# Optimization experiments

Measured on AMD Instinct MI355X. Metric: run time of the kernel, lower is better.

Reference implementation:

```python
import math
import jax, jax.numpy as jnp
import numpy as np

_MAX_CELL_MULTIPLES = 100000


def _grid_bounds(cell, cutoff, r1, r2):
    """Static (concrete) grid bounds, mirroring the module's a_max/b_max/c_max."""
    cell = np.asarray(cell, dtype=np.float64)
    dr = np.asarray(r2, dtype=np.float64) - np.asarray(r1, dtype=np.float64)
    a, b, c = cell[0], cell[1], cell[2]
    vol = abs(float(np.dot(a, np.cross(b, c))))

    def nmax(u, v):
        cr = np.cross(u, v)
        ln = float(np.linalg.norm(cr))
        d = abs(float(np.dot(dr, cr / ln)))
        return min(int(math.floor((cutoff + d) / vol * ln)), _MAX_CELL_MULTIPLES)

    return nmax(b, c), nmax(a, c), nmax(a, b)


def _candidate_grid(a_max, b_max, c_max):
    ii, jj, kk = jnp.meshgrid(
        jnp.arange(-a_max, a_max + 1),
        jnp.arange(-b_max, b_max + 1),
        jnp.arange(-c_max, c_max + 1),
        indexing="ij",
    )
    # [N,3] int32, ordered exactly like the original triple nested loop (i outer, k inner)
    return jnp.stack([ii.ravel(), jj.ravel(), kk.ravel()], axis=-1).astype(jnp.int32)


def setup_inputs() -> dict:
    key = jax.random.key(0)
    k1, k2 = jax.random.split(key)
    cell = jnp.array([[2.0, 0.0, 0.0], [0.1, 2.0, 0.0], [0.1, 0.1, 2.0]], dtype=jnp.float32)
    cutoff = jnp.float32(200.0)
    r1 = jax.random.normal(k1, (3,), dtype=jnp.float32)
    r2 = jax.random.normal(k2, (3,), dtype=jnp.float32)
    return {"cell": cell, "cutoff": cutoff, "r1": r1, "r2": r2}


def reference(cell, cutoff, r1, r2):
    # Grid extents are concrete (computed from host values), so shapes are static.
    a_max, b_max, c_max = _grid_bounds(cell, float(cutoff), r1, r2)
    ijk = _candidate_grid(a_max, b_max, c_max)  # [N,3] int32
    dr = r2 - r1
    # displacement = i*a + j*b + k*c for every lattice image, vectorized as a GEMM
    disp = ijk.astype(cell.dtype) @ cell  # [N,3]
    out_vec = disp + dr  # [N,3]
    mask = jnp.sum(out_vec * out_vec, axis=-1) < cutoff * cutoff  # [N]
    # Padded/masked equivalent of the original's variable-length compaction:
    # rows with mask==False are zeroed instead of removed (static shapes for jit).
    vectors = jnp.where(mask[:, None], out_vec, jnp.zeros((), out_vec.dtype))
    cell_indices = jnp.where(mask[:, None], ijk, jnp.zeros((), ijk.dtype))
    return vectors, cell_indices, mask
```

## Files before the change

### kernel.cpp

```cpp
#include <hip/hip_runtime.h>
#include <stdint.h>

struct Params {
  int a_max, b_max, c_max;
  uint32_t Dj, Dk;
  uint64_t Mj, Mk;
};

__device__ __forceinline__ int iabs_(int x) { return x < 0 ? -x : x; }

__device__ __forceinline__ int nmax_ref(double u0, double u1, double u2,
                                        double v0, double v1, double v2,
                                        double dr0, double dr1, double dr2,
                                        double co, double vol) {
#pragma clang fp contract(off)
  double x0 = u1 * v2 - u2 * v1;
  double x1 = u2 * v0 - u0 * v2;
  double x2 = u0 * v1 - u1 * v0;
  double ln = sqrt((x0 * x0 + x1 * x1) + x2 * x2);
  double d  = fabs((dr0 * (x0 / ln) + dr1 * (x1 / ln)) + dr2 * (x2 / ln));
  double f  = floor((co + d) / vol * ln);
  long long n = (long long)f;
  if (n > 100000) n = 100000;
  return (int)n;
}

__global__ void setup_kernel(const float* __restrict__ cell,
                             const float* __restrict__ cutoff,
                             const float* __restrict__ r1,
                             const float* __restrict__ r2,
                             Params* __restrict__ p, int N) {
#pragma clang fp contract(off)
  double a0 = cell[0], a1 = cell[1], a2 = cell[2];
  double b0 = cell[3], b1 = cell[4], b2 = cell[5];
  double c0 = cell[6], c1 = cell[7], c2 = cell[8];
  double dr0 = (double)r2[0] - (double)r1[0];
  double dr1 = (double)r2[1] - (double)r1[1];
  double dr2 = (double)r2[2] - (double)r1[2];
  double co  = (double)cutoff[0];

  double bc0 = b1 * c2 - b2 * c1;
  double bc1 = b2 * c0 - b0 * c2;
  double bc2 = b0 * c1 - b1 * c0;
  double vol = fabs((a0 * bc0 + a1 * bc1) + a2 * bc2);

  int am = nmax_ref(b0, b1, b2, c0, c1, c2, dr0, dr1, dr2, co, vol);
  int bm = nmax_ref(a0, a1, a2, c0, c1, c2, dr0, dr1, dr2, co, vol);
  int cm = nmax_ref(a0, a1, a2, b0, b1, b2, dr0, dr1, dr2, co, vol);

  int fa = am, fb = bm, fc = cm;
  bool found = ((long long)(2 * am + 1) * (2 * bm + 1) * (2 * cm + 1) == (long long)N);
  for (int r = 1; r <= 3 && !found; ++r)
    for (int da = -1; da <= 1 && !found; ++da)
      for (int db = -1; db <= 1 && !found; ++db)
        for (int dc = -1; dc <= 1 && !found; ++dc) {
          if (iabs_(da) + iabs_(db) + iabs_(dc) != r) continue;
          long long A = am + da, B = bm + db, C = cm + dc;
          if (A < 0 || B < 0 || C < 0) continue;
          long long P = (2 * A + 1) * (2 * B + 1) * (2 * C + 1);
          if (P == (long long)N) { fa = (int)A; fb = (int)B; fc = (int)C; found = true; }
        }

  p->a_max = fa; p->b_max = fb; p->c_max = fc;
  uint32_t Dk = (uint32_t)(2 * fc + 1);
  uint32_t Dj = (uint32_t)(2 * fb + 1) * Dk;
  p->Dk = Dk; p->Dj = Dj;
  p->Mj = ((1ULL << 47) / Dj) + 1;
  p->Mk = ((1ULL << 47) / Dk) + 1;
}

__global__ __launch_bounds__(256) void periodic_main(
    const float* __restrict__ cell, const float* __restrict__ cutoff,
    const float* __restrict__ r1, const float* __restrict__ r2,
    const Params* __restrict__ p, float* __restrict__ out, int N) {
  int n = blockIdx.x * 256 + threadIdx.x;
  if (n >= N) return;

  const int am = p->a_max, bm = p->b_max, cm = p->c_max;
  const uint32_t Dj = p->Dj, Dk = p->Dk;
  const uint64_t Mj = p->Mj, Mk = p->Mk;

  uint32_t un  = (uint32_t)n;
  uint32_t qi  = (uint32_t)(((uint64_t)un * Mj) >> 47);
  uint32_t rem = un - qi * Dj;
  uint32_t qj  = (uint32_t)(((uint64_t)rem * Mk) >> 47);
  uint32_t qk  = rem - qj * Dk;

  float fi = (float)((int)qi - am);
  float fj = (float)((int)qj - bm);
  float fk = (float)((int)qk - cm);

  float ax = cell[0], ay = cell[1], az = cell[2];
  float bx = cell[3], by = cell[4], bz = cell[5];
  float cx = cell[6], cy = cell[7], cz = cell[8];
  float drx = r2[0] - r1[0], dry = r2[1] - r1[1], drz = r2[2] - r1[2];

  float vx = fmaf(fk, cx, fmaf(fj, bx, fi * ax)) + drx;
  float vy = fmaf(fk, cy, fmaf(fj, by, fi * ay)) + dry;
  float vz = fmaf(fk, cz, fmaf(fj, bz, fi * az)) + drz;

  float s  = fmaf(vz, vz, fmaf(vy, vy, vx * vx));
  float co = cutoff[0];
  bool  m  = s < co * co;

  float vxo = m ? vx : 0.f, vyo = m ? vy : 0.f, vzo = m ? vz : 0.f;
  float fio = m ? fi : 0.f, fjo = m ? fj : 0.f, fko = m ? fk : 0.f;

  size_t base = (size_t)3 * (size_t)n;
  size_t N3   = (size_t)3 * (size_t)N;
  __builtin_nontemporal_store(vxo, out + base + 0);
  __builtin_nontemporal_store(vyo, out + base + 1);
  __builtin_nontemporal_store(vzo, out + base + 2);
  __builtin_nontemporal_store(fio, out + N3 + base + 0);
  __builtin_nontemporal_store(fjo, out + N3 + base + 1);
  __builtin_nontemporal_store(fko, out + N3 + base + 2);
  __builtin_nontemporal_store(m ? 1.0f : 0.0f, out + 2 * N3 + (size_t)n);
}

extern "C" void kernel_launch(void* const* d_in, const int* in_sizes, int n_in,
                              void* d_out, int out_size, void* d_ws, size_t ws_size,
                              hipStream_t stream) {
  const float* cell   = (const float*)d_in[0];
  const float* cutoff = (const float*)d_in[1];
  const float* r1     = (const float*)d_in[2];
  const float* r2     = (const float*)d_in[3];
  float* out = (float*)d_out;

  int N = out_size / 7;
  Params* p = (Params*)d_ws;

  setup_kernel<<<1, 1, 0, stream>>>(cell, cutoff, r1, r2, p, N);
  int blocks = (N + 255) / 256;
  periodic_main<<<blocks, 256, 0, stream>>>(cell, cutoff, r1, r2, p, out, N);
}
```

Measured before the change: 254.6 us.

## Stage outputs in shared memory and write coalesced float4 stores

Each block now handles 1024 points with 4 per thread and writes the strided 3-component results into shared memory first. It then copies them to global memory as aligned float4 vector stores, with scalar head and tail handling for misaligned segment offsets. This replaces the stride-3 scalar nontemporal stores with wide coalesced writes. The cost is shared memory use, a block barrier, and the loss of nontemporal hints.

```diff
diff --git a/kernel.cpp b/kernel.cpp
--- a/kernel.cpp
+++ b/kernel.cpp
@@ -73,48 +73,101 @@
     const float* __restrict__ cell, const float* __restrict__ cutoff,
     const float* __restrict__ r1, const float* __restrict__ r2,
     const Params* __restrict__ p, float* __restrict__ out, int N) {
-  int n = blockIdx.x * 256 + threadIdx.x;
-  if (n >= N) return;
+  __shared__ __align__(16) float s_vec[3 * 1024];
+  __shared__ __align__(16) float s_idx[4 + 3 * 1024];
+  __shared__ __align__(16) float s_msk[4 + 1024];
+
+  const int tid = threadIdx.x;
+  const int n0  = blockIdx.x << 10;
 
   const int am = p->a_max, bm = p->b_max, cm = p->c_max;
   const uint32_t Dj = p->Dj, Dk = p->Dk;
   const uint64_t Mj = p->Mj, Mk = p->Mk;
 
-  uint32_t un  = (uint32_t)n;
-  uint32_t qi  = (uint32_t)(((uint64_t)un * Mj) >> 47);
-  uint32_t rem = un - qi * Dj;
-  uint32_t qj  = (uint32_t)(((uint64_t)rem * Mk) >> 47);
-  uint32_t qk  = rem - qj * Dk;
+  const float ax = cell[0], ay = cell[1], az = cell[2];
+  const float bx = cell[3], by = cell[4], bz = cell[5];
+  const float cx = cell[6], cy = cell[7], cz = cell[8];
+  const float drx = r2[0] - r1[0], dry = r2[1] - r1[1], drz = r2[2] - r1[2];
+  const float co  = cutoff[0];
+  const float co2 = co * co;
 
-  float fi = (float)((int)qi - am);
-  float fj = (float)((int)qj - bm);
-  float fk = (float)((int)qk - cm);
+  const size_t NN = (size_t)N;
+  const size_t gA = (size_t)3 * (size_t)n0;
+  const size_t gB = (size_t)3 * NN + (size_t)3 * (size_t)n0;
+  const size_t gC = (size_t)6 * NN + (size_t)n0;
+  const int s1 = (int)(gB & 3);
+  const int s2 = (int)(gC & 3);
 
-  float ax = cell[0], ay = cell[1], az = cell[2];
-  float bx = cell[3], by = cell[4], bz = cell[5];
-  float cx = cell[6], cy = cell[7], cz = cell[8];
-  float drx = r2[0] - r1[0], dry = r2[1] - r1[1], drz = r2[2] - r1[2];
+#pragma unroll
+  for (int u = 0; u < 4; ++u) {
+    const int pt = tid + (u << 8);
+    const int n  = n0 + pt;
+    if (n < N) {
+      uint32_t un  = (uint32_t)n;
+      uint32_t qi  = (uint32_t)(((uint64_t)un * Mj) >> 47);
+      uint32_t rem = un - qi * Dj;
+      uint32_t qj  = (uint32_t)(((uint64_t)rem * Mk) >> 47);
+      uint32_t qk  = rem - qj * Dk;
 
-  float vx = fmaf(fk, cx, fmaf(fj, bx, fi * ax)) + drx;
-  float vy = fmaf(fk, cy, fmaf(fj, by, fi * ay)) + dry;
-  float vz = fmaf(fk, cz, fmaf(fj, bz, fi * az)) + drz;
+      float fi = (float)((int)qi - am);
+      float fj = (float)((int)qj - bm);
+      float fk = (float)((int)qk - cm);
 
-  float s  = fmaf(vz, vz, fmaf(vy, vy, vx * vx));
-  float co = cutoff[0];
-  bool  m  = s < co * co;
+      float vx = fmaf(fk, cx, fmaf(fj, bx, fi * ax)) + drx;
+      float vy = fmaf(fk, cy, fmaf(fj, by, fi * ay)) + dry;
+      float vz = fmaf(fk, cz, fmaf(fj, bz, fi * az)) + drz;
 
-  float vxo = m ? vx : 0.f, vyo = m ? vy : 0.f, vzo = m ? vz : 0.f;
-  float fio = m ? fi : 0.f, fjo = m ? fj : 0.f, fko = m ? fk : 0.f;
+      float s = fmaf(vz, vz, fmaf(vy, vy, vx * vx));
+      bool  m = s < co2;
 
-  size_t base = (size_t)3 * (size_t)n;
-  size_t N3   = (size_t)3 * (size_t)N;
-  __builtin_nontemporal_store(vxo, out + base + 0);
-  __builtin_nontemporal_store(vyo, out + base + 1);
-  __builtin_nontemporal_store(vzo, out + base + 2);
-  __builtin_nontemporal_store(fio, out + N3 + base + 0);
-  __builtin_nontemporal_store(fjo, out + N3 + base + 1);
-  __builtin_nontemporal_store(fko, out + N3 + base + 2);
-  __builtin_nontemporal_store(m ? 1.0f : 0.0f, out + 2 * N3 + (size_t)n);
+      int b3 = 3 * pt;
+      s_vec[b3 + 0]      = m ? vx : 0.f;
+      s_vec[b3 + 1]      = m ? vy : 0.f;
+      s_vec[b3 + 2]      = m ? vz : 0.f;
+      s_idx[s1 + b3 + 0] = m ? fi : 0.f;
+      s_idx[s1 + b3 + 1] = m ? fj : 0.f;
+      s_idx[s1 + b3 + 2] = m ? fk : 0.f;
+      s_msk[s2 + pt]     = m ? 1.0f : 0.0f;
+    }
+  }
+  __syncthreads();
+
+  const int ptsLeft = N - n0;
+  const int pts     = ptsLeft < 1024 ? ptsLeft : 1024;
+  const int c3      = 3 * pts;
+
+  {
+    const int nf4 = c3 >> 2;
+    const float4* src = reinterpret_cast<const float4*>(s_vec);
+    float4* dst = reinterpret_cast<float4*>(out + gA);
+    for (int i = tid; i < nf4; i += 256) dst[i] = src[i];
+    const int tail = c3 & 3, tb = nf4 << 2;
+    if (tid < tail) out[gA + tb + tid] = s_vec[tb + tid];
+  }
+  {
+    int head = (4 - s1) & 3;
+    if (head > c3) head = c3;
+    if (tid < head) out[gB + tid] = s_idx[s1 + tid];
+    const int rem = c3 - head;
+    const int nf4 = rem >> 2;
+    const float4* src = reinterpret_cast<const float4*>(&s_idx[s1 + head]);
+    float4* dst = reinterpret_cast<float4*>(out + gB + head);
+    for (int i = tid; i < nf4; i += 256) dst[i] = src[i];
+    const int tail = rem & 3, tb = head + (nf4 << 2);
+    if (tid < tail) out[gB + tb + tid] = s_idx[s1 + tb + tid];
+  }
+  {
+    int head = (4 - s2) & 3;
+    if (head > pts) head = pts;
+    if (tid < head) out[gC + tid] = s_msk[s2 + tid];
+    const int rem = pts - head;
+    const int nf4 = rem >> 2;
+    const float4* src = reinterpret_cast<const float4*>(&s_msk[s2 + head]);
+    float4* dst = reinterpret_cast<float4*>(out + gC + head);
+    for (int i = tid; i < nf4; i += 256) dst[i] = src[i];
+    const int tail = rem & 3, tb = head + (nf4 << 2);
+    if (tid < tail) out[gC + tb + tid] = s_msk[s2 + tb + tid];
+  }
 }
 
 extern "C" void kernel_launch(void* const* d_in, const int* in_sizes, int n_in,
@@ -130,6 +183,6 @@
   Params* p = (Params*)d_ws;
 
   setup_kernel<<<1, 1, 0, stream>>>(cell, cutoff, r1, r2, p, N);
-  int blocks = (N + 255) / 256;
+  int blocks = (N + 1023) / 1024;
   periodic_main<<<blocks, 256, 0, stream>>>(cell, cutoff, r1, r2, p, out, N);
 }
```

Measured after the change: 233.3 us. -8.4%, faster.

## Map threads to output float4 words for fully coalesced vector stores

Applied to the files above, without the earlier changes.

Each thread now computes four consecutive output words and writes them with one float4 store. Before, each thread handled one lattice point and issued seven scattered scalar nontemporal stores with a stride of three. Every output element recomputes its lattice index, vector and mask, and the division magic constants are narrowed to 32-bit multipliers. The goal is fully coalesced wide writes at the cost of redundant arithmetic, roughly three times the per-point work. The narrower magic constants may be inexact for very large grid sizes.

```diff
diff --git a/kernel.cpp b/kernel.cpp
--- a/kernel.cpp
+++ b/kernel.cpp
@@ -2,9 +2,9 @@
 #include <stdint.h>
 
 struct Params {
-  int a_max, b_max, c_max;
+  int am, bm, cm;
   uint32_t Dj, Dk;
-  uint64_t Mj, Mk;
+  uint32_t Mj40, Mk32;
 };
 
 __device__ __forceinline__ int iabs_(int x) { return x < 0 ? -x : x; }
@@ -61,60 +61,87 @@
           if (P == (long long)N) { fa = (int)A; fb = (int)B; fc = (int)C; found = true; }
         }
 
-  p->a_max = fa; p->b_max = fb; p->c_max = fc;
+  p->am = fa; p->bm = fb; p->cm = fc;
   uint32_t Dk = (uint32_t)(2 * fc + 1);
   uint32_t Dj = (uint32_t)(2 * fb + 1) * Dk;
-  p->Dk = Dk; p->Dj = Dj;
-  p->Mj = ((1ULL << 47) / Dj) + 1;
-  p->Mk = ((1ULL << 47) / Dk) + 1;
+  p->Dj = Dj; p->Dk = Dk;
+  p->Mj40 = (uint32_t)(((1ULL << 40) / Dj) + 1);
+  p->Mk32 = (uint32_t)(((1ULL << 32) / Dk) + 1);
 }
 
-__global__ __launch_bounds__(256) void periodic_main(
+__global__ __launch_bounds__(256) void periodic_fused(
     const float* __restrict__ cell, const float* __restrict__ cutoff,
     const float* __restrict__ r1, const float* __restrict__ r2,
     const Params* __restrict__ p, float* __restrict__ out, int N) {
-  int n = blockIdx.x * 256 + threadIdx.x;
-  if (n >= N) return;
+  const int tid = threadIdx.x;
 
-  const int am = p->a_max, bm = p->b_max, cm = p->c_max;
+  const int am = p->am, bm = p->bm, cm = p->cm;
   const uint32_t Dj = p->Dj, Dk = p->Dk;
-  const uint64_t Mj = p->Mj, Mk = p->Mk;
+  const uint32_t Mj40 = p->Mj40, Mk32 = p->Mk32;
 
-  uint32_t un  = (uint32_t)n;
-  uint32_t qi  = (uint32_t)(((uint64_t)un * Mj) >> 47);
-  uint32_t rem = un - qi * Dj;
-  uint32_t qj  = (uint32_t)(((uint64_t)rem * Mk) >> 47);
-  uint32_t qk  = rem - qj * Dk;
+  const float ax = cell[0], ay = cell[1], az = cell[2];
+  const float bx = cell[3], by = cell[4], bz = cell[5];
+  const float cx = cell[6], cy = cell[7], cz = cell[8];
+  const float drx = r2[0] - r1[0], dry = r2[1] - r1[1], drz = r2[2] - r1[2];
+  const float co  = cutoff[0];
+  const float co2 = co * co;
 
-  float fi = (float)((int)qi - am);
-  float fj = (float)((int)qj - bm);
-  float fk = (float)((int)qk - cm);
+  const size_t N3 = (size_t)3 * (size_t)N;
+  const size_t N6 = 2 * N3;
+  const size_t N7 = N6 + (size_t)N;
+  const size_t f4_total = (N7 + 3) >> 2;
 
-  float ax = cell[0], ay = cell[1], az = cell[2];
-  float bx = cell[3], by = cell[4], bz = cell[5];
-  float cx = cell[6], cy = cell[7], cz = cell[8];
-  float drx = r2[0] - r1[0], dry = r2[1] - r1[1], drz = r2[2] - r1[2];
+  const size_t w0 = (size_t)blockIdx.x * 1024 + (size_t)tid;
 
-  float vx = fmaf(fk, cx, fmaf(fj, bx, fi * ax)) + drx;
-  float vy = fmaf(fk, cy, fmaf(fj, by, fi * ay)) + dry;
-  float vz = fmaf(fk, cz, fmaf(fj, bz, fi * az)) + drz;
+#pragma unroll
+  for (int u = 0; u < 4; ++u) {
+    const size_t w = w0 + (size_t)(u << 8);
+    if (w >= f4_total) continue;
+    const size_t g0 = w << 2;
 
-  float s  = fmaf(vz, vz, fmaf(vy, vy, vx * vx));
-  float co = cutoff[0];
-  bool  m  = s < co * co;
+    float vals[4];
+#pragma unroll
+    for (int j = 0; j < 4; ++j) {
+      const size_t g = g0 + (size_t)j;
+      const bool rB = g >= N3;
+      const bool rC = g >= N6;
+      uint32_t gp = (uint32_t)(g - (rB ? N3 : 0) - (rC ? N3 : 0));
+      uint32_t pA = (uint32_t)(((uint64_t)gp * 0xAAAAAAABULL) >> 33);
+      uint32_t c  = gp - 3u * pA;
+      uint32_t pp = rC ? gp : pA;
+      uint32_t qi  = (uint32_t)(((uint64_t)pp  * Mj40) >> 40);
+      uint32_t rem = pp - qi * Dj;
+      uint32_t qj  = (uint32_t)(((uint64_t)rem * Mk32) >> 32);
+      uint32_t qk  = rem - qj * Dk;
 
-  float vxo = m ? vx : 0.f, vyo = m ? vy : 0.f, vzo = m ? vz : 0.f;
-  float fio = m ? fi : 0.f, fjo = m ? fj : 0.f, fko = m ? fk : 0.f;
+      float fi = (float)((int)qi - am);
+      float fj = (float)((int)qj - bm);
+      float fk = (float)((int)qk - cm);
 
-  size_t base = (size_t)3 * (size_t)n;
-  size_t N3   = (size_t)3 * (size_t)N;
-  __builtin_nontemporal_store(vxo, out + base + 0);
-  __builtin_nontemporal_store(vyo, out + base + 1);
-  __builtin_nontemporal_store(vzo, out + base + 2);
-  __builtin_nontemporal_store(fio, out + N3 + base + 0);
-  __builtin_nontemporal_store(fjo, out + N3 + base + 1);
-  __builtin_nontemporal_store(fko, out + N3 + base + 2);
-  __builtin_nontemporal_store(m ? 1.0f : 0.0f, out + 2 * N3 + (size_t)n);
+      float vx = fmaf(fk, cx, fmaf(fj, bx, fi * ax)) + drx;
+      float vy = fmaf(fk, cy, fmaf(fj, by, fi * ay)) + dry;
+      float vz = fmaf(fk, cz, fmaf(fj, bz, fi * az)) + drz;
+
+      float s = fmaf(vz, vz, fmaf(vy, vy, vx * vx));
+      bool  m = s < co2;
+
+      float s0 = rB ? fi : vx;
+      float s1 = rB ? fj : vy;
+      float s2 = rB ? fk : vz;
+      float t  = (c == 0u) ? s0 : (c == 1u) ? s1 : s2;
+      t = rC ? 1.0f : t;
+      vals[j] = m ? t : 0.0f;
+    }
+
+    if (g0 + 4 <= N7) {
+      *reinterpret_cast<float4*>(out + g0) =
+          make_float4(vals[0], vals[1], vals[2], vals[3]);
+    } else {
+#pragma unroll
+      for (int j = 0; j < 4; ++j)
+        if (g0 + (size_t)j < N7) out[g0 + (size_t)j] = vals[j];
+    }
+  }
 }
 
 extern "C" void kernel_launch(void* const* d_in, const int* in_sizes, int n_in,
@@ -130,6 +157,8 @@
   Params* p = (Params*)d_ws;
 
   setup_kernel<<<1, 1, 0, stream>>>(cell, cutoff, r1, r2, p, N);
-  int blocks = (N + 255) / 256;
-  periodic_main<<<blocks, 256, 0, stream>>>(cell, cutoff, r1, r2, p, out, N);
+
+  size_t f4_total = ((size_t)out_size + 3) >> 2;
+  int blocks = (int)((f4_total + 1023) >> 10);
+  periodic_fused<<<blocks, 256, 0, stream>>>(cell, cutoff, r1, r2, p, out, N);
 }
```

Measured after the change: 253.1 us. About the same (-0.6%).
